# Performance work log

Measured on AMD Instinct MI355X. Metric: run time of the kernel, lower is better.

The kernel has to match this reference:

```python
import jax, jax.numpy as jnp
import numpy as np

# ---- static config (matches init_kwargs) ----
B, CIN, H, W = 32, 64, 32, 32
CO, K, G, PAD = 64, 7, 8, 3
R_RAMP = 3.0            # ramp size R
Z_INIT = 4.0            # initial adaptive-span value
MAXSZ = W // 2          # adaptive_mask max_size = image_size/2 = 16
CPG = CO // G           # channels per group


def _unfold(t, k):
    # torch x.unfold(2,k,1).unfold(3,k,1): [B,C,Hp,Wp] -> [B,C,Ho,Wo,kh,kw]
    ho = t.shape[2] - k + 1
    wo = t.shape[3] - k + 1
    return jnp.stack(
        [jnp.stack([t[:, :, i:i + ho, j:j + wo] for j in range(k)], axis=-1)
         for i in range(k)], axis=-2)


def _adaptive_mask(current_val):
    # AdaptiveMask.forward applied to [B,G,CPG,H,W]; x.shape[-1] == W.
    # one_d_mask[g, i] is the soft value written on 'ring' i (rows i and W-1-i,
    # columns spanning the ring interval) of a WxW mask.
    template = jnp.linspace(1.0 - MAXSZ, 0.0, MAXSZ)            # [MAXSZ]
    om = (template[None, :] + current_val * MAXSZ) / R_RAMP + 1.0
    om = jnp.clip(om, 0.0, 1.0)                                  # [G, MAXSZ]
    # (slice [-(W//2):] is identity since MAXSZ == W//2)
    i = jnp.arange(W)
    r = jnp.minimum(i, W - 1 - i)                                # ring index per row
    top = i <= (W - 1 - i)
    lo = jnp.where(top, r, r + 1)    # bottom row of ring misses its leftmost col
    hi = W - 1 - r
    c = jnp.arange(W)
    in_ring = (c[None, :] >= lo[:, None]) & (c[None, :] <= hi[:, None])  # [W,W]
    vals = om[:, r]                                              # [G, W]
    return jnp.where(in_ring[None, :, :], vals[:, :, None], 1.0)  # [G,W,W]


def setup_inputs() -> dict:
    key = jax.random.key(0)
    ks = jax.random.split(key, 6)
    x = jax.random.normal(ks[0], (B, CIN, H, W), dtype=jnp.float32)
    fan_out_std = np.sqrt(2.0 / CO).astype(np.float32)  # kaiming fan_out, 1x1 conv
    w_q = jax.random.normal(ks[1], (CO, CIN), dtype=jnp.float32) * fan_out_std
    w_k = jax.random.normal(ks[2], (CO, CIN), dtype=jnp.float32) * fan_out_std
    w_v = jax.random.normal(ks[3], (CO, CIN), dtype=jnp.float32) * fan_out_std
    rel_h = jax.random.normal(ks[4], (CO // 2, 1, 1, K, 1), dtype=jnp.float32)
    rel_w = jax.random.normal(ks[5], (CO // 2, 1, 1, 1, K), dtype=jnp.float32)
    current_val = jnp.full((G, 1), Z_INIT, dtype=jnp.float32)
    return {"x": x, "w_q": w_q, "w_k": w_k, "w_v": w_v,
            "rel_h": rel_h, "rel_w": rel_w, "current_val": current_val}


def reference(x, w_q, w_k, w_v, rel_h, rel_w, current_val):
    q = jnp.einsum('bchw,oc->bohw', x, w_q)                       # [B,CO,H,W]
    xp = jnp.pad(x, ((0, 0), (0, 0), (PAD, PAD), (PAD, PAD)))
    k = jnp.einsum('bchw,oc->bohw', xp, w_k)
    v = jnp.einsum('bchw,oc->bohw', xp, w_v)
    k = _unfold(k, K)                                             # [B,CO,H,W,K,K]
    v = _unfold(v, K)
    k_h, k_w = jnp.split(k, 2, axis=1)
    k = jnp.concatenate([k_h + rel_h, k_w + rel_w], axis=1)
    k = k.reshape(B, G, CPG, H, W, K * K)
    v = v.reshape(B, G, CPG, H, W, K * K)
    q = q.reshape(B, G, CPG, H, W, 1)
    scores = jnp.sum(q * k, axis=2)                               # [B,G,H,W,K*K]
    attn = jax.nn.softmax(scores, axis=-1)
    out = jnp.sum(attn[:, :, None] * v, axis=-1)                  # [B,G,CPG,H,W]
    mask = _adaptive_mask(current_val)                            # [G,W,W]
    return out * mask[None, :, None, :, :]
```

## Files before the change

kernel.cpp:

```cpp
#include <hip/hip_runtime.h>

#define BB    32
#define CINc  64
#define HHc   32
#define WWc   32
#define COc   64
#define KSc   7
#define GGc   8
#define PADc  3
#define CPGc  8
#define NPIX  (HHc * WWc)

typedef _Float16 h8    __attribute__((ext_vector_type(8)));
typedef _Float16 h2    __attribute__((ext_vector_type(2)));
typedef float    f32x4 __attribute__((ext_vector_type(4)));

#if defined(__has_builtin)
#if __has_builtin(__builtin_amdgcn_fdot2)
#define HAVE_FDOT2 1
#endif
#endif

__global__ __launch_bounds__(1024, 4) void fused_kernel(
    const float* __restrict__ x,
    const float* __restrict__ wq,
    const float* __restrict__ wk,
    const float* __restrict__ wv,
    const float* __restrict__ rel_h,
    const float* __restrict__ rel_w,
    const float* __restrict__ cv,
    float* __restrict__ out)
{
    __shared__ __attribute__((aligned(16))) f32x4 kplv[NPIX];
    __shared__ __attribute__((aligned(16))) f32x4 vplv[NPIX];
    __shared__ __attribute__((aligned(16))) f32x4 qplv[NPIX];

    const int bi  = blockIdx.x;
    const int xcd = bi & 7;
    const int t   = bi >> 3;
    const int im  = t & 3;
    const int g   = t >> 2;
    const int b   = im * 8 + xcd;
    const int o0  = g * CPGc;
    const int tid = threadIdx.x;
    const int w   = tid & 31;
    const int h   = tid >> 5;

    const int lane = tid & 63;
    const int wp   = (tid >> 6) << 6;
    const int an   = lane & 15;
    const int quad = lane >> 4;

    const float* xb = x + (size_t)b * CINc * NPIX;

    h8 bf[2][2];
    {
        const float* br0 = (an < 8) ? (wk + (o0 + an) * CINc)
                                    : (wv + (o0 + an - 8) * CINc);
        const float* br1 = wq + (o0 + ((an < 8) ? an : 0)) * CINc;
#pragma unroll
        for (int ks = 0; ks < 2; ++ks) {
            const int c0 = ks * 32 + quad * 8;
#pragma unroll
            for (int jj = 0; jj < 8; ++jj) {
                bf[0][ks][jj] = (_Float16)br0[c0 + jj];
                bf[1][ks][jj] = (_Float16)br1[c0 + jj];
            }
        }
    }

    f32x4 acc0[4], acc1[4];
#pragma unroll
    for (int m = 0; m < 4; ++m) { acc0[m] = (f32x4)0.f; acc1[m] = (f32x4)0.f; }

#pragma unroll
    for (int m = 0; m < 4; ++m) {
        const float* xpx = xb + wp + m * 16 + an;
#pragma unroll
        for (int ks = 0; ks < 2; ++ks) {
            const int c0 = ks * 32 + quad * 8;
            h8 a;
#pragma unroll
            for (int jj = 0; jj < 8; ++jj)
                a[jj] = (_Float16)xpx[(c0 + jj) * NPIX];
            acc0[m] = __builtin_amdgcn_mfma_f32_16x16x32_f16(a, bf[0][ks], acc0[m], 0, 0, 0);
            acc1[m] = __builtin_amdgcn_mfma_f32_16x16x32_f16(a, bf[1][ks], acc1[m], 0, 0, 0);
        }
    }

    {
        _Float16* kp16 = (_Float16*)kplv;
        _Float16* qp16 = (_Float16*)qplv;
        _Float16* vp16 = (_Float16*)vplv;
#pragma unroll
        for (int m = 0; m < 4; ++m) {
#pragma unroll
            for (int r = 0; r < 4; ++r) {
                const int pix = wp + m * 16 + quad * 4 + r;
                const float d0 = acc0[m][r];
                if (an < 8) {
                    kp16[pix * 8 + an] = (_Float16)d0;
                    qp16[pix * 8 + an] = (_Float16)acc1[m][r];
                } else {
                    vp16[pix * 8 + (an - 8)] = (_Float16)d0;
                }
            }
        }
    }

    __syncthreads();

    f32x4 qraw = qplv[tid];
    const h2* qh = (const h2*)&qraw;
    h2 q2[4] = {qh[0], qh[1], qh[2], qh[3]};
    float qf[CPGc];
#pragma unroll
    for (int jj = 0; jj < 4; ++jj) {
        qf[2 * jj]     = (float)q2[jj].x;
        qf[2 * jj + 1] = (float)q2[jj].y;
    }

    const bool use_h = (g < 4);
    const float* relp = use_h ? (rel_h + o0 * KSc) : (rel_w + (o0 - 32) * KSc);
    float qrel[KSc];
#pragma unroll
    for (int tt = 0; tt < KSc; ++tt) {
        float s = 0.f;
#pragma unroll
        for (int oi = 0; oi < CPGc; ++oi)
            s = fmaf(qf[oi], relp[oi * KSc + tt], s);
        qrel[tt] = s;
    }

    int  xcl[KSc];
    bool xin[KSc];
#pragma unroll
    for (int kj = 0; kj < KSc; ++kj) {
        const int xx = w + kj - PADc;
        xin[kj] = (xx >= 0) && (xx < WWc);
        xcl[kj] = min(max(xx, 0), WWc - 1);
    }

    float den = 0.f;
    float acc[CPGc];
#pragma unroll
    for (int oi = 0; oi < CPGc; ++oi) acc[oi] = 0.f;

#pragma unroll
    for (int ki = 0; ki < KSc; ++ki) {
        const int y    = h + ki - PADc;
        const bool yin = (y >= 0) && (y < HHc);
        const int base = min(max(y, 0), HHc - 1) * WWc;
#pragma unroll
        for (int kj = 0; kj < KSc; ++kj) {
            const int p = base + xcl[kj];
            const f32x4 kraw = kplv[p];
            const f32x4 vraw = vplv[p];
            const bool in = yin && xin[kj];

            float d = 0.f;
            const h2* kh = (const h2*)&kraw;
            const h2* vh = (const h2*)&vraw;
#if HAVE_FDOT2
            d = __builtin_amdgcn_fdot2(q2[0], kh[0], d, false);
            d = __builtin_amdgcn_fdot2(q2[1], kh[1], d, false);
            d = __builtin_amdgcn_fdot2(q2[2], kh[2], d, false);
            d = __builtin_amdgcn_fdot2(q2[3], kh[3], d, false);
#else
#pragma unroll
            for (int jj = 0; jj < 4; ++jj) {
                d = fmaf(qf[2 * jj],     (float)kh[jj].x, d);
                d = fmaf(qf[2 * jj + 1], (float)kh[jj].y, d);
            }
#endif
            const float s = (use_h ? qrel[ki] : qrel[kj]) + (in ? d : 0.f);
            const float e = __expf(s);
            den += e;
            const float ev = in ? e : 0.f;
            acc[0] = fmaf(ev, (float)vh[0].x, acc[0]);
            acc[1] = fmaf(ev, (float)vh[0].y, acc[1]);
            acc[2] = fmaf(ev, (float)vh[1].x, acc[2]);
            acc[3] = fmaf(ev, (float)vh[1].y, acc[3]);
            acc[4] = fmaf(ev, (float)vh[2].x, acc[4]);
            acc[5] = fmaf(ev, (float)vh[2].y, acc[5]);
            acc[6] = fmaf(ev, (float)vh[3].x, acc[6]);
            acc[7] = fmaf(ev, (float)vh[3].y, acc[7]);
        }
    }

    const int  r  = min(h, HHc - 1 - h);
    const int  lo = (h <= HHc - 1 - h) ? r : r + 1;
    const int  hi = HHc - 1 - r;
    const bool in_ring = (w >= lo) && (w <= hi);
    const float cvg = cv[g];
    float om = ((float)r - 15.0f + cvg * 16.0f) * (1.0f / 3.0f) + 1.0f;
    om = fminf(fmaxf(om, 0.0f), 1.0f);
    const float maskv = in_ring ? om : 1.0f;
    const float scale = maskv / den;

    float* ob = out + ((size_t)b * COc + o0) * NPIX + tid;
#pragma unroll
    for (int oi = 0; oi < CPGc; ++oi)
        ob[(size_t)oi * NPIX] = acc[oi] * scale;
}

extern "C" void kernel_launch(void* const* d_in, const int* in_sizes, int n_in,
                              void* d_out, int out_size, void* d_ws, size_t ws_size,
                              hipStream_t stream) {
    const float* x     = (const float*)d_in[0];
    const float* wq    = (const float*)d_in[1];
    const float* wk    = (const float*)d_in[2];
    const float* wv    = (const float*)d_in[3];
    const float* rel_h = (const float*)d_in[4];
    const float* rel_w = (const float*)d_in[5];
    const float* cv    = (const float*)d_in[6];
    float* out = (float*)d_out;

    fused_kernel<<<256, 1024, 0, stream>>>(x, wq, wk, wv, rel_h, rel_w, cv, out);
}
```

Measured before the change: 87.17 us.

## Split each image-group block into two row halves with halo recomputation

Each block now handles half of the image rows (16 output rows) for one batch/group, so the launch becomes 512 blocks of 512 threads instead of 256 blocks of 1024. Each half recomputes the K/V/Q projections for 19 rows, which covers the 3-row halo needed by the 7x7 window. Shared memory per block shrinks to 640 positions. The aim is more, smaller blocks for better occupancy and load balance across CUs. The cost is redundant projection work on the halo rows and an uneven projection loop, since 10 tiles are spread over 8 waves.

New measurement: 87.69 us. No clear change (+0.6%).

```diff
diff --git a/kernel.cpp b/kernel.cpp
--- a/kernel.cpp
+++ b/kernel.cpp
@@ -10,6 +10,9 @@
 #define PADc  3
 #define CPGc  8
 #define NPIX  (HHc * WWc)
+#define HROWS 19
+#define NPOSH (HROWS * 32)
+#define NPOSP 640
 
 typedef _Float16 h8    __attribute__((ext_vector_type(8)));
 typedef _Float16 h2    __attribute__((ext_vector_type(2)));
@@ -21,7 +24,7 @@
 #endif
 #endif
 
-__global__ __launch_bounds__(1024, 4) void fused_kernel(
+__global__ __launch_bounds__(512, 4) void fused_kernel(
     const float* __restrict__ x,
     const float* __restrict__ wq,
     const float* __restrict__ wk,
@@ -31,23 +34,26 @@
     const float* __restrict__ cv,
     float* __restrict__ out)
 {
-    __shared__ __attribute__((aligned(16))) f32x4 kplv[NPIX];
-    __shared__ __attribute__((aligned(16))) f32x4 vplv[NPIX];
-    __shared__ __attribute__((aligned(16))) f32x4 qplv[NPIX];
-
-    const int bi  = blockIdx.x;
-    const int xcd = bi & 7;
-    const int t   = bi >> 3;
-    const int im  = t & 3;
-    const int g   = t >> 2;
-    const int b   = im * 8 + xcd;
-    const int o0  = g * CPGc;
-    const int tid = threadIdx.x;
-    const int w   = tid & 31;
-    const int h   = tid >> 5;
+    __shared__ __attribute__((aligned(16))) f32x4 kplv[NPOSP];
+    __shared__ __attribute__((aligned(16))) f32x4 vplv[NPOSP];
+    __shared__ __attribute__((aligned(16))) f32x4 qplv[NPOSP];
+
+    const int bi   = blockIdx.x;
+    const int xcd  = bi & 7;
+    const int t0   = bi >> 3;
+    const int im   = t0 & 3;
+    const int rest = t0 >> 2;
+    const int g    = rest >> 1;
+    const int hf   = rest & 1;
+    const int b    = im * 8 + xcd;
+    const int o0   = g * CPGc;
+    const int tid  = threadIdx.x;
+
+    const int rowbase = hf ? (HHc - HROWS) : 0;
+    const int pgbase  = rowbase * WWc;
 
     const int lane = tid & 63;
-    const int wp   = (tid >> 6) << 6;
+    const int wid  = tid >> 6;
     const int an   = lane & 15;
     const int quad = lane >> 4;
 
@@ -69,40 +75,45 @@
         }
     }
 
-    f32x4 acc0[4], acc1[4];
-#pragma unroll
-    for (int m = 0; m < 4; ++m) { acc0[m] = (f32x4)0.f; acc1[m] = (f32x4)0.f; }
-
-#pragma unroll
-    for (int m = 0; m < 4; ++m) {
-        const float* xpx = xb + wp + m * 16 + an;
-#pragma unroll
-        for (int ks = 0; ks < 2; ++ks) {
-            const int c0 = ks * 32 + quad * 8;
-            h8 a;
-#pragma unroll
-            for (int jj = 0; jj < 8; ++jj)
-                a[jj] = (_Float16)xpx[(c0 + jj) * NPIX];
-            acc0[m] = __builtin_amdgcn_mfma_f32_16x16x32_f16(a, bf[0][ks], acc0[m], 0, 0, 0);
-            acc1[m] = __builtin_amdgcn_mfma_f32_16x16x32_f16(a, bf[1][ks], acc1[m], 0, 0, 0);
-        }
-    }
-
-    {
-        _Float16* kp16 = (_Float16*)kplv;
-        _Float16* qp16 = (_Float16*)qplv;
-        _Float16* vp16 = (_Float16*)vplv;
+    _Float16* kp16 = (_Float16*)kplv;
+    _Float16* qp16 = (_Float16*)qplv;
+    _Float16* vp16 = (_Float16*)vplv;
+
+#pragma unroll 1
+    for (int tt = wid; tt < 10; tt += 8) {
+        const int pbase = pgbase + tt * 64;
+
+        f32x4 acc0[4], acc1[4];
+#pragma unroll
+        for (int m = 0; m < 4; ++m) { acc0[m] = (f32x4)0.f; acc1[m] = (f32x4)0.f; }
+
 #pragma unroll
         for (int m = 0; m < 4; ++m) {
+            const int pg = min(pbase + m * 16 + an, NPIX - 1);
+            const float* xpx = xb + pg;
+#pragma unroll
+            for (int ks = 0; ks < 2; ++ks) {
+                const int c0 = ks * 32 + quad * 8;
+                h8 a;
+#pragma unroll
+                for (int jj = 0; jj < 8; ++jj)
+                    a[jj] = (_Float16)xpx[(c0 + jj) * NPIX];
+                acc0[m] = __builtin_amdgcn_mfma_f32_16x16x32_f16(a, bf[0][ks], acc0[m], 0, 0, 0);
+                acc1[m] = __builtin_amdgcn_mfma_f32_16x16x32_f16(a, bf[1][ks], acc1[m], 0, 0, 0);
+            }
+        }
+
+#pragma unroll
+        for (int m = 0; m < 4; ++m) {
 #pragma unroll
             for (int r = 0; r < 4; ++r) {
-                const int pix = wp + m * 16 + quad * 4 + r;
+                const int lp = tt * 64 + m * 16 + quad * 4 + r;
                 const float d0 = acc0[m][r];
                 if (an < 8) {
-                    kp16[pix * 8 + an] = (_Float16)d0;
-                    qp16[pix * 8 + an] = (_Float16)acc1[m][r];
+                    kp16[lp * 8 + an] = (_Float16)d0;
+                    qp16[lp * 8 + an] = (_Float16)acc1[m][r];
                 } else {
-                    vp16[pix * 8 + (an - 8)] = (_Float16)d0;
+                    vp16[lp * 8 + (an - 8)] = (_Float16)d0;
                 }
             }
         }
@@ -110,7 +121,11 @@
 
     __syncthreads();
 
-    f32x4 qraw = qplv[tid];
+    const int w  = tid & 31;
+    const int lh = tid >> 5;
+    const int h  = hf * 16 + lh;
+
+    f32x4 qraw = qplv[(h - rowbase) * WWc + w];
     const h2* qh = (const h2*)&qraw;
     h2 q2[4] = {qh[0], qh[1], qh[2], qh[3]};
     float qf[CPGc];
@@ -150,7 +165,7 @@
     for (int ki = 0; ki < KSc; ++ki) {
         const int y    = h + ki - PADc;
         const bool yin = (y >= 0) && (y < HHc);
-        const int base = min(max(y, 0), HHc - 1) * WWc;
+        const int base = (min(max(y, 0), HHc - 1) - rowbase) * WWc;
 #pragma unroll
         for (int kj = 0; kj < KSc; ++kj) {
             const int p = base + xcl[kj];
@@ -198,7 +213,7 @@
     const float maskv = in_ring ? om : 1.0f;
     const float scale = maskv / den;
 
-    float* ob = out + ((size_t)b * COc + o0) * NPIX + tid;
+    float* ob = out + ((size_t)b * COc + o0) * NPIX + h * WWc + w;
 #pragma unroll
     for (int oi = 0; oi < CPGc; ++oi)
         ob[(size_t)oi * NPIX] = acc[oi] * scale;
@@ -216,5 +231,5 @@
     const float* cv    = (const float*)d_in[6];
     float* out = (float*)d_out;
 
-    fused_kernel<<<256, 1024, 0, stream>>>(x, wq, wk, wv, rel_h, rel_w, cv, out);
+    fused_kernel<<<512, 512, 0, stream>>>(x, wq, wk, wv, rel_h, rel_w, cv, out);
 }
```
